# Kernel tuning notes

Hardware: AMD Instinct MI355X
Metric: run time of the kernel (lower is better)

The kernel has to match this reference:

```python
import jax, jax.numpy as jnp
import numpy as np

COMMITMENT = 0.25
THRESHOLD = 0.6
SNR_DB = 30.0  # eval_snr_db default-ish channel condition (fixed for determinism)
LN_EPS = 1e-5


def _layernorm(x, g, b):
    m = jnp.mean(x, axis=-1, keepdims=True)
    v = jnp.var(x, axis=-1, keepdims=True)
    return (x - m) * jax.lax.rsqrt(v + LN_EPS) * g + b


def _vq(x, codebook):
    # x: [T, D], codebook: [K, D]. Nearest-neighbor quantize + per-token VQ loss + STE.
    d = (x * x).sum(-1, keepdims=True) - 2.0 * (x @ codebook.T) + (codebook * codebook).sum(-1)  # [T, K]
    idx = jnp.argmin(d, axis=-1)
    q = codebook[idx]  # [T, D]
    loss = (COMMITMENT * jnp.mean((x - jax.lax.stop_gradient(q)) ** 2, axis=-1)
            + jnp.mean((jax.lax.stop_gradient(x) - q) ** 2, axis=-1))  # [T]
    q_ste = x + jax.lax.stop_gradient(q - x)
    return q_ste, loss


def setup_inputs() -> dict:
    key = jax.random.key(0)
    ks = jax.random.split(key, 8)
    B, N, De, Dq, Dd = 64, 196, 768, 512, 256
    return {
        'x_tokens': jax.random.normal(ks[0], (B, N, De), jnp.float32),
        'fim_logits': jax.random.normal(ks[1], (B, N, 1), jnp.float32),
        'W_proj': jax.random.normal(ks[2], (De, Dq), jnp.float32) * (1.0 / np.sqrt(De)),
        'b_proj': jnp.zeros((Dq,), jnp.float32),
        'ln_g': jnp.ones((Dq,), jnp.float32),
        'ln_b': jnp.zeros((Dq,), jnp.float32),
        'cb_high': jax.random.normal(ks[3], (4096, Dq), jnp.float32),
        'cb_low': jax.random.normal(ks[4], (256, Dq), jnp.float32),
        'W_dec': jax.random.normal(ks[5], (Dq, Dd), jnp.float32) * (1.0 / np.sqrt(Dq)),
        'b_dec': jnp.zeros((Dd,), jnp.float32),
        'h_ri': jax.random.normal(ks[6], (B, 2), jnp.float32),
        'noise': jax.random.normal(ks[7], (B, N, Dq), jnp.float32),
    }


def reference(x_tokens, fim_logits, W_proj, b_proj, ln_g, ln_b, cb_high, cb_low, W_dec, b_dec, h_ri, noise):
    B, N, _ = x_tokens.shape
    score = jax.nn.sigmoid(fim_logits[..., 0])          # [B, N]
    route_high = score > THRESHOLD                       # [B, N] bool

    x_proj = _layernorm(x_tokens @ W_proj + b_proj, ln_g, ln_b)  # [B, N, Dq]
    D = x_proj.shape[-1]
    xf = x_proj.reshape(-1, D)
    mf = route_high.reshape(-1)
    sf = score.reshape(-1)

    # Compute both experts densely, select with mask (same math as the masked
    # gather/scatter dispatch in the torch code, jit-friendly static shapes).
    q_high, loss_high = _vq(xf, cb_high)
    q_low, loss_low = _vq(xf, cb_low)
    final = jnp.where(mf[:, None], q_high, q_low).reshape(B, N, D)

    n_high = jnp.maximum(mf.sum(), 1)
    n_low = jnp.maximum((~mf).sum(), 1)
    vq_loss = (jnp.sum(jnp.where(mf, loss_high * sf, 0.0)) / n_high
               + jnp.sum(jnp.where(mf, 0.0, loss_low * (1.0 - sf))) / n_low) / 2.0

    # Rayleigh channel: per-sample fading magnitude h = |CN(0,1)|/sqrt(2), AWGN, equalize.
    n_var = 10.0 ** (-SNR_DB / 10.0)
    h = jnp.sqrt((h_ri ** 2).sum(-1)) / jnp.sqrt(2.0)    # [B]
    h = h[:, None, None]
    y = (h * final + jnp.sqrt(n_var) * noise) / h

    x_dec = y @ W_dec + b_dec                            # [B, N, 256]
    return x_dec, vq_loss
```

## Files before the change

kernel.cpp:

```cpp
#include <hip/hip_runtime.h>
#include <math.h>

#define T_TOK 12544
#define DE 768
#define DQ 512
#define DD 256
#define SEQ 196
#define NCH 4096
#define NCL 256
#define SPL_H 16
#define CODES_PER_BLK 256
#define MARGIN 2.0f
#define CAND_CAP 16
#define VQTOK 32

typedef __attribute__((ext_vector_type(8))) short s16x8;
typedef __attribute__((ext_vector_type(4))) float f32x4;

__device__ __forceinline__ float wave_reduce_sum(float v) {
    #pragma unroll
    for (int off = 32; off > 0; off >>= 1) v += __shfl_xor(v, off);
    return v;
}

__device__ __forceinline__ unsigned short f2bf(float f) {
    unsigned int u = __float_as_uint(f);
    u = (u + 0x7fffu + ((u >> 16) & 1u)) >> 16;
    return (unsigned short)u;
}
__device__ __forceinline__ float bf2f(unsigned short h) {
    return __uint_as_float(((unsigned int)h) << 16);
}

__device__ __forceinline__ void gload_lds16(const unsigned short* g, unsigned short* l) {
    __builtin_amdgcn_global_load_lds(
        (const __attribute__((address_space(1))) void*)g,
        (__attribute__((address_space(3))) void*)l,
        16, 0, 0);
}

__device__ __forceinline__ void sumsq_body(const float* __restrict__ cb,
                                           float* __restrict__ cs2,
                                           unsigned short* __restrict__ cbB,
                                           int blk, int NC) {
    int row = blk * 4 + (threadIdx.x >> 6);
    int lane = threadIdx.x & 63;
    if (row >= NC) return;
    const float4* p = (const float4*)(cb + (size_t)row * DQ);
    float4 a = p[lane];
    float4 b = p[lane + 64];
    if (cbB) {
        unsigned short* dst = cbB + (size_t)row * DQ;
        ushort4 ha, hb;
        ha.x = f2bf(a.x); ha.y = f2bf(a.y); ha.z = f2bf(a.z); ha.w = f2bf(a.w);
        hb.x = f2bf(b.x); hb.y = f2bf(b.y); hb.z = f2bf(b.z); hb.w = f2bf(b.w);
        *(ushort4*)(dst + lane * 4) = ha;
        *(ushort4*)(dst + 256 + lane * 4) = hb;
    }
    float s = a.x*a.x + a.y*a.y + a.z*a.z + a.w*a.w
            + b.x*b.x + b.y*b.y + b.z*b.z + b.w*b.w;
    s = wave_reduce_sum(s);
    if (lane == 0) cs2[row] = s;
}

__device__ __forceinline__ void split_body(const float* __restrict__ W, int K, int N,
                                           unsigned short* __restrict__ Thi,
                                           unsigned short* __restrict__ Tlo,
                                           int blk, int nb) {
    int total = K * N;
    for (int idx = blk * 256 + threadIdx.x; idx < total; idx += nb * 256) {
        int n = idx / K, k = idx - n * K;
        float v = W[(size_t)k * N + n];
        unsigned short h = f2bf(v);
        Thi[idx] = h;
        Tlo[idx] = f2bf(v - bf2f(h));
    }
}

__global__ __launch_bounds__(256) void prep_all(const float* __restrict__ cb_h,
                                                float* __restrict__ cs2h,
                                                unsigned short* __restrict__ cbhB,
                                                const float* __restrict__ cb_l,
                                                float* __restrict__ cs2l,
                                                unsigned short* __restrict__ cblB,
                                                const float* __restrict__ Wp,
                                                unsigned short* __restrict__ WThi,
                                                unsigned short* __restrict__ WTlo,
                                                const float* __restrict__ Wd,
                                                unsigned short* __restrict__ WdThi,
                                                unsigned short* __restrict__ WdTlo) {
    int blk = blockIdx.x;
    if (blk < 1024)       sumsq_body(cb_h, cs2h, cbhB, blk, NCH);
    else if (blk < 1088)  sumsq_body(cb_l, cs2l, cblB, blk - 1024, NCL);
    else if (blk < 1600)  split_body(Wp, DE, DQ, WThi, WTlo, blk - 1088, 512);
    else                  split_body(Wd, DQ, DD, WdThi, WdTlo, blk - 1600, 256);
}

template<int NC>
__global__ __launch_bounds__(256) void code_sumsq(const float* __restrict__ cb,
                                                  float* __restrict__ cs2) {
    sumsq_body(cb, cs2, nullptr, blockIdx.x, NC);
}

template<int KDIM, int NSTRIDE>
__global__ __launch_bounds__(256) void gemm_mfma3_128(const float* __restrict__ A,
                                                      const unsigned short* __restrict__ BThi,
                                                      const unsigned short* __restrict__ BTlo,
                                                      const float* __restrict__ bias,
                                                      float* __restrict__ out) {
    __shared__ __align__(16) unsigned short Ahi[128 * 32];
    __shared__ __align__(16) unsigned short Alo[128 * 32];
    __shared__ __align__(16) unsigned short Bhi[128 * 32];
    __shared__ __align__(16) unsigned short Blo[128 * 32];
    const int m0 = blockIdx.x * 128, n0 = blockIdx.y * 128;
    const int tid = threadIdx.x, lane = tid & 63, w = tid >> 6;
    const int wr = w >> 1, wc = w & 1;
    const int arow = tid >> 1, ahalf = tid & 1;

    const int cb0 = w * 2, cb1 = w * 2 + 1;
    const int gcol0 = n0 + cb0 * 16 + (lane >> 2);
    const int gcol1 = n0 + cb1 * 16 + (lane >> 2);
    const int ch0 = (lane & 3) ^ ((gcol0 >> 1) & 3);
    const int ch1 = (lane & 3) ^ ((gcol1 >> 1) & 3);
    const unsigned short* sH0 = BThi + (size_t)gcol0 * KDIM + ch0 * 8;
    const unsigned short* sH1 = BThi + (size_t)gcol1 * KDIM + ch1 * 8;
    const unsigned short* sL0 = BTlo + (size_t)gcol0 * KDIM + ch0 * 8;
    const unsigned short* sL1 = BTlo + (size_t)gcol1 * KDIM + ch1 * 8;

    f32x4 acc[4][4] = {};
    const int NT = KDIM / 32;
    for (int t = 0; t < NT; t++) {
        const int k0 = t * 32;
        gload_lds16(sH0 + k0, Bhi + cb0 * 512);
        gload_lds16(sH1 + k0, Bhi + cb1 * 512);
        gload_lds16(sL0 + k0, Blo + cb0 * 512);
        gload_lds16(sL1 + k0, Blo + cb1 * 512);
        {
            const float* src = A + (size_t)(m0 + arow) * KDIM + k0 + ahalf * 16;
            float4 v0 = *(const float4*)(src + 0);
            float4 v1 = *(const float4*)(src + 4);
            float4 v2 = *(const float4*)(src + 8);
            float4 v3 = *(const float4*)(src + 12);
            float xv[16] = {v0.x,v0.y,v0.z,v0.w, v1.x,v1.y,v1.z,v1.w,
                            v2.x,v2.y,v2.z,v2.w, v3.x,v3.y,v3.z,v3.w};
            const int swzA = (arow >> 1) & 3;
            #pragma unroll
            for (int cc = 0; cc < 2; cc++) {
                unsigned int hw[4], lw[4];
                #pragma unroll
                for (int j = 0; j < 4; j++) {
                    float f0 = xv[cc*8 + 2*j], f1 = xv[cc*8 + 2*j + 1];
                    unsigned short h0 = f2bf(f0), h1 = f2bf(f1);
                    unsigned short l0 = f2bf(f0 - bf2f(h0));
                    unsigned short l1 = f2bf(f1 - bf2f(h1));
                    hw[j] = (unsigned)h0 | ((unsigned)h1 << 16);
                    lw[j] = (unsigned)l0 | ((unsigned)l1 << 16);
                }
                int c = ahalf * 2 + cc;
                int doff = arow * 32 + (c ^ swzA) * 8;
                *(uint4*)&Ahi[doff] = make_uint4(hw[0], hw[1], hw[2], hw[3]);
                *(uint4*)&Alo[doff] = make_uint4(lw[0], lw[1], lw[2], lw[3]);
            }
        }
        __syncthreads();
        const int fr = lane & 15, fs = lane >> 4;
        s16x8 ah[4], al[4];
        #pragma unroll
        for (int tm = 0; tm < 4; tm++) {
            int row = wr * 64 + tm * 16 + fr;
            int off = row * 32 + (fs ^ ((row >> 1) & 3)) * 8;
            ah[tm] = *(const s16x8*)&Ahi[off];
            al[tm] = *(const s16x8*)&Alo[off];
        }
        #pragma unroll
        for (int tn = 0; tn < 4; tn++) {
            int col = wc * 64 + tn * 16 + fr;
            int boff = col * 32 + (fs ^ ((col >> 1) & 3)) * 8;
            s16x8 bh = *(const s16x8*)&Bhi[boff];
            s16x8 bl = *(const s16x8*)&Blo[boff];
            #pragma unroll
            for (int tm = 0; tm < 4; tm++) {
                acc[tm][tn] = __builtin_amdgcn_mfma_f32_16x16x32_bf16(ah[tm], bh, acc[tm][tn], 0, 0, 0);
                acc[tm][tn] = __builtin_amdgcn_mfma_f32_16x16x32_bf16(ah[tm], bl, acc[tm][tn], 0, 0, 0);
                acc[tm][tn] = __builtin_amdgcn_mfma_f32_16x16x32_bf16(al[tm], bh, acc[tm][tn], 0, 0, 0);
            }
        }
        __syncthreads();
    }
    const int fr = lane & 15, fg = lane >> 4;
    #pragma unroll
    for (int tn = 0; tn < 4; tn++) {
        const int col = n0 + wc * 64 + tn * 16 + fr;
        const float bb = bias[col];
        #pragma unroll
        for (int tm = 0; tm < 4; tm++) {
            #pragma unroll
            for (int r = 0; r < 4; r++) {
                int row = m0 + wr * 64 + tm * 16 + fg * 4 + r;
                out[(size_t)row * NSTRIDE + col] = acc[tm][tn][r] + bb;
            }
        }
    }
}

template<int KDIM, int NSTRIDE, int BN>
__global__ __launch_bounds__(256) void gemm_mfma3(const float* __restrict__ A,
                                                  const unsigned short* __restrict__ BThi,
                                                  const unsigned short* __restrict__ BTlo,
                                                  const float* __restrict__ bias,
                                                  float* __restrict__ out) {
    constexpr int CPW = BN / 64;
    __shared__ __align__(16) unsigned short Ahi[2][64 * 32];
    __shared__ __align__(16) unsigned short Alo[2][64 * 32];
    __shared__ __align__(16) unsigned short Bhi[2][BN * 32];
    __shared__ __align__(16) unsigned short Blo[2][BN * 32];
    const int m0 = blockIdx.x * 64, n0 = blockIdx.y * BN;
    const int tid = threadIdx.x, lane = tid & 63, w = tid >> 6;
    const int stok = tid >> 2, sslot = tid & 3;

    f32x4 acc[4][CPW] = {};
    float4 av0, av1;
    uint4 bh4[CPW], bl4[CPW];

    auto loadStep = [&](int k0) {
        const float* src = A + (size_t)(m0 + stok) * KDIM + k0 + sslot * 8;
        av0 = *(const float4*)src;
        av1 = *(const float4*)(src + 4);
        #pragma unroll
        for (int c = 0; c < CPW; c++) {
            size_t soff = (size_t)(n0 + c * 64 + stok) * KDIM + k0 + sslot * 8;
            bh4[c] = *(const uint4*)(BThi + soff);
            bl4[c] = *(const uint4*)(BTlo + soff);
        }
    };
    auto writeStep = [&](int buf) {
        float xv[8] = {av0.x, av0.y, av0.z, av0.w, av1.x, av1.y, av1.z, av1.w};
        unsigned int hw[4], lw[4];
        #pragma unroll
        for (int j = 0; j < 4; j++) {
            unsigned short h0 = f2bf(xv[2*j]),   h1 = f2bf(xv[2*j+1]);
            unsigned short l0 = f2bf(xv[2*j] - bf2f(h0));
            unsigned short l1 = f2bf(xv[2*j+1] - bf2f(h1));
            hw[j] = (unsigned)h0 | ((unsigned)h1 << 16);
            lw[j] = (unsigned)l0 | ((unsigned)l1 << 16);
        }
        int doffA = stok * 32 + (sslot ^ ((stok >> 1) & 3)) * 8;
        *(uint4*)&Ahi[buf][doffA] = make_uint4(hw[0], hw[1], hw[2], hw[3]);
        *(uint4*)&Alo[buf][doffA] = make_uint4(lw[0], lw[1], lw[2], lw[3]);
        #pragma unroll
        for (int c = 0; c < CPW; c++) {
            int col = c * 64 + stok;
            int doffB = col * 32 + (sslot ^ ((col >> 1) & 3)) * 8;
            *(uint4*)&Bhi[buf][doffB] = bh4[c];
            *(uint4*)&Blo[buf][doffB] = bl4[c];
        }
    };

    loadStep(0); writeStep(0); __syncthreads();
    const int NT = KDIM / 32;
    for (int t = 0; t < NT; t++) {
        const int cur = t & 1;
        if (t + 1 < NT) loadStep((t + 1) * 32);
        const int fr = lane & 15, fs = lane >> 4;
        s16x8 ah[4], al[4];
        #pragma unroll
        for (int tm = 0; tm < 4; tm++) {
            int tok = tm * 16 + fr;
            int off = tok * 32 + (fs ^ ((tok >> 1) & 3)) * 8;
            ah[tm] = *(const s16x8*)&Ahi[cur][off];
            al[tm] = *(const s16x8*)&Alo[cur][off];
        }
        #pragma unroll
        for (int n = 0; n < CPW; n++) {
            int col = w * (16 * CPW) + n * 16 + fr;
            int boff = col * 32 + (fs ^ ((col >> 1) & 3)) * 8;
            s16x8 bh = *(const s16x8*)&Bhi[cur][boff];
            s16x8 bl = *(const s16x8*)&Blo[cur][boff];
            #pragma unroll
            for (int tm = 0; tm < 4; tm++) {
                acc[tm][n] = __builtin_amdgcn_mfma_f32_16x16x32_bf16(ah[tm], bh, acc[tm][n], 0, 0, 0);
                acc[tm][n] = __builtin_amdgcn_mfma_f32_16x16x32_bf16(ah[tm], bl, acc[tm][n], 0, 0, 0);
                acc[tm][n] = __builtin_amdgcn_mfma_f32_16x16x32_bf16(al[tm], bh, acc[tm][n], 0, 0, 0);
            }
        }
        if (t + 1 < NT) writeStep(cur ^ 1);
        __syncthreads();
    }
    const int fr = lane & 15, fg = lane >> 4;
    #pragma unroll
    for (int n = 0; n < CPW; n++) {
        const int col = n0 + w * (16 * CPW) + n * 16 + fr;
        const float bb = bias[col];
        #pragma unroll
        for (int tm = 0; tm < 4; tm++) {
            #pragma unroll
            for (int r = 0; r < 4; r++) {
                int row = m0 + tm * 16 + fg * 4 + r;
                out[(size_t)row * NSTRIDE + col] = acc[tm][n][r] + bb;
            }
        }
    }
}

__global__ __launch_bounds__(256) void proj_gemm(const float* __restrict__ X,
                                                 const float* __restrict__ W,
                                                 const float* __restrict__ bias,
                                                 float* __restrict__ out) {
    __shared__ float As[32][66];
    __shared__ float Bs[32][64];
    const int m0 = blockIdx.x * 64, n0 = blockIdx.y * 64;
    const int tid = threadIdx.x;
    const int tx = tid & 15, ty = tid >> 4;
    float acc[4][4] = {};
    for (int k0 = 0; k0 < DE; k0 += 32) {
        {
            int e = tid;
            int r = e >> 3, c4 = e & 7;
            float4 v = *(const float4*)(X + (size_t)(m0 + r) * DE + k0 + c4 * 4);
            As[c4*4+0][r] = v.x; As[c4*4+1][r] = v.y; As[c4*4+2][r] = v.z; As[c4*4+3][r] = v.w;
            e = tid + 256;
            r = e >> 3; c4 = e & 7;
            v = *(const float4*)(X + (size_t)(m0 + r) * DE + k0 + c4 * 4);
            As[c4*4+0][r] = v.x; As[c4*4+1][r] = v.y; As[c4*4+2][r] = v.z; As[c4*4+3][r] = v.w;
        }
        {
            int e = tid;
            int kk = e >> 4, c4 = e & 15;
            *(float4*)&Bs[kk][c4*4] = *(const float4*)(W + (size_t)(k0 + kk) * DQ + n0 + c4 * 4);
            e = tid + 256;
            kk = e >> 4; c4 = e & 15;
            *(float4*)&Bs[kk][c4*4] = *(const float4*)(W + (size_t)(k0 + kk) * DQ + n0 + c4 * 4);
        }
        __syncthreads();
        #pragma unroll
        for (int k = 0; k < 32; k++) {
            float2 a01 = *(const float2*)&As[k][ty * 4];
            float2 a23 = *(const float2*)&As[k][ty * 4 + 2];
            float4 b = *(const float4*)&Bs[k][tx * 4];
            float av[4] = {a01.x, a01.y, a23.x, a23.y};
            float bv[4] = {b.x, b.y, b.z, b.w};
            #pragma unroll
            for (int i = 0; i < 4; i++)
                #pragma unroll
                for (int j = 0; j < 4; j++)
                    acc[i][j] += av[i] * bv[j];
        }
        __syncthreads();
    }
    float4 bv4 = *(const float4*)(bias + n0 + tx * 4);
    float bb[4] = {bv4.x, bv4.y, bv4.z, bv4.w};
    #pragma unroll
    for (int i = 0; i < 4; i++) {
        int row = m0 + ty * 4 + i;
        float4 o;
        o.x = acc[i][0] + bb[0];
        o.y = acc[i][1] + bb[1];
        o.z = acc[i][2] + bb[2];
        o.w = acc[i][3] + bb[3];
        *(float4*)(out + (size_t)row * DQ + n0 + tx * 4) = o;
    }
}

__global__ __launch_bounds__(256) void ln_route(float* __restrict__ xp,
                                                const float* __restrict__ g,
                                                const float* __restrict__ b,
                                                const float* __restrict__ logits,
                                                float* __restrict__ score,
                                                int* __restrict__ mask,
                                                unsigned short* __restrict__ xpB) {
    int row = blockIdx.x * 4 + (threadIdx.x >> 6);
    int lane = threadIdx.x & 63;
    float* p = xp + (size_t)row * DQ;
    float4 v0 = *(float4*)(p + lane * 4);
    float4 v1 = *(float4*)(p + 256 + lane * 4);
    float s  = v0.x + v0.y + v0.z + v0.w + v1.x + v1.y + v1.z + v1.w;
    float ss = v0.x*v0.x + v0.y*v0.y + v0.z*v0.z + v0.w*v0.w
             + v1.x*v1.x + v1.y*v1.y + v1.z*v1.z + v1.w*v1.w;
    s = wave_reduce_sum(s);
    ss = wave_reduce_sum(ss);
    float m = s * (1.f / DQ);
    float var = ss * (1.f / DQ) - m * m;
    float scale = rsqrtf(var + 1e-5f);
    float4 g0 = *(const float4*)(g + lane * 4);
    float4 g1 = *(const float4*)(g + 256 + lane * 4);
    float4 b0 = *(const float4*)(b + lane * 4);
    float4 b1 = *(const float4*)(b + 256 + lane * 4);
    float4 o0, o1;
    o0.x = (v0.x - m) * scale * g0.x + b0.x;
    o0.y = (v0.y - m) * scale * g0.y + b0.y;
    o0.z = (v0.z - m) * scale * g0.z + b0.z;
    o0.w = (v0.w - m) * scale * g0.w + b0.w;
    o1.x = (v1.x - m) * scale * g1.x + b1.x;
    o1.y = (v1.y - m) * scale * g1.y + b1.y;
    o1.z = (v1.z - m) * scale * g1.z + b1.z;
    o1.w = (v1.w - m) * scale * g1.w + b1.w;
    *(float4*)(p + lane * 4) = o0;
    *(float4*)(p + 256 + lane * 4) = o1;
    if (xpB) {
        unsigned short* dst = xpB + (size_t)row * DQ;
        ushort4 h0, h1;
        h0.x = f2bf(o0.x); h0.y = f2bf(o0.y); h0.z = f2bf(o0.z); h0.w = f2bf(o0.w);
        h1.x = f2bf(o1.x); h1.y = f2bf(o1.y); h1.z = f2bf(o1.z); h1.w = f2bf(o1.w);
        *(ushort4*)(dst + lane * 4) = h0;
        *(ushort4*)(dst + 256 + lane * 4) = h1;
    }
    if (lane == 0) {
        float lg = logits[row];
        float sc = 1.f / (1.f + expf(-lg));
        score[row] = sc;
        mask[row] = sc > 0.6f ? 1 : 0;
    }
}

__global__ __launch_bounds__(1024) void scan_compact(const int* __restrict__ mask,
                                                     int* __restrict__ hlist,
                                                     int* __restrict__ llist,
                                                     int* __restrict__ counts) {
    __shared__ int wsum[16];
    __shared__ int base_h, base_l;
    int tid = threadIdx.x, lane = tid & 63, wid = tid >> 6;
    if (tid == 0) { base_h = 0; base_l = 0; }
    __syncthreads();
    for (int t0 = 0; t0 < T_TOK; t0 += 1024) {
        int t = t0 + tid;
        int valid = t < T_TOK;
        int m = valid ? mask[t] : 0;
        unsigned long long bal = __ballot(m);
        int pre = __popcll(bal & ((1ull << lane) - 1ull));
        if (lane == 0) wsum[wid] = __popcll(bal);
        __syncthreads();
        int woff = 0;
        for (int w = 0; w < wid; w++) woff += wsum[w];
        int btot = 0;
        for (int w = 0; w < 16; w++) btot += wsum[w];
        int vcnt = T_TOK - t0; if (vcnt > 1024) vcnt = 1024;
        int bh = base_h, bl = base_l;
        if (valid) {
            if (m) hlist[bh + woff + pre] = t;
            else   llist[bl + (tid - (woff + pre))] = t;
        }
        __syncthreads();
        if (tid == 0) { base_h = bh + btot; base_l = bl + (vcnt - btot); }
        __syncthreads();
    }
    if (tid == 0) { counts[0] = base_h; counts[1] = base_l; }
}

__global__ __launch_bounds__(256) void vq_mfma_all(const unsigned short* __restrict__ xpB,
                                                   const unsigned short* __restrict__ cbhB,
                                                   const float* __restrict__ cs2h,
                                                   const int* __restrict__ hlist,
                                                   const unsigned short* __restrict__ cblB,
                                                   const float* __restrict__ cs2l,
                                                   const int* __restrict__ llist,
                                                   const int* __restrict__ counts,
                                                   float* __restrict__ smaxH,
                                                   int* __restrict__ scntH,
                                                   uint2* __restrict__ candH,
                                                   float* __restrict__ smaxL,
                                                   int* __restrict__ scntL,
                                                   uint2* __restrict__ candL) {
    const int by = blockIdx.y;
    const unsigned short* cbB; const float* cs2; const int* list;
    float* smax; int* scnt; uint2* cand;
    int count, slice, SPLIT;
    if (by < SPL_H) {
        cbB = cbhB; cs2 = cs2h; list = hlist; count = counts[0];
        slice = by; SPLIT = SPL_H; smax = smaxH; scnt = scntH; cand = candH;
    } else {
        cbB = cblB; cs2 = cs2l; list = llist; count = counts[1];
        slice = 0; SPLIT = 1; smax = smaxL; scnt = scntL; cand = candL;
    }
    const int base = blockIdx.x * VQTOK;
    if (base >= count) return;
    const int cbase = slice * CODES_PER_BLK;

    __shared__ __align__(16) unsigned short Abuf[VQTOK * 32];
    __shared__ __align__(16) unsigned short Bbuf[256 * 32];
    __shared__ float wmaxs[4][VQTOK];
    __shared__ float tokmax[VQTOK];
    __shared__ int ccnt[VQTOK];
    __shared__ uint2 cland[VQTOK][CAND_CAP];
    __shared__ int rows_s[VQTOK];

    const int tid = threadIdx.x;
    const int lane = tid & 63;
    const int w = tid >> 6;
    const int stok = tid >> 2, sslot = tid & 3;

    if (tid < VQTOK) {
        int tl = base + tid;
        rows_s[tid] = list[tl < count ? tl : (count - 1)];
        ccnt[tid] = 0;
    }
    __syncthreads();

    const int swz = sslot ^ ((stok >> 1) & 3);
    const unsigned short* gA  = xpB + (size_t)rows_s[stok & (VQTOK - 1)] * DQ + swz * 8;
    const unsigned short* gB0 = cbB + (size_t)(cbase + 0 * 64 + stok) * DQ + swz * 8;
    const unsigned short* gB1 = cbB + (size_t)(cbase + 1 * 64 + stok) * DQ + swz * 8;
    const unsigned short* gB2 = cbB + (size_t)(cbase + 2 * 64 + stok) * DQ + swz * 8;
    const unsigned short* gB3 = cbB + (size_t)(cbase + 3 * 64 + stok) * DQ + swz * 8;
    unsigned short* dA = Abuf + w * 512;
    unsigned short* dB = Bbuf + w * 512;

    f32x4 acc[2][4] = {};

    const int NT = DQ / 32;
    for (int t = 0; t < NT; t++) {
        const int k0 = t * 32;
        if (w < 2) gload_lds16(gA + k0, dA);
        gload_lds16(gB0 + k0, dB + 0 * 2048);
        gload_lds16(gB1 + k0, dB + 1 * 2048);
        gload_lds16(gB2 + k0, dB + 2 * 2048);
        gload_lds16(gB3 + k0, dB + 3 * 2048);
        __syncthreads();
        const int fr = lane & 15, fs = lane >> 4;
        s16x8 af[2], bf[4];
        #pragma unroll
        for (int tm = 0; tm < 2; tm++) {
            int tok = tm * 16 + fr;
            af[tm] = *(const s16x8*)&Abuf[tok * 32 + (fs ^ ((tok >> 1) & 3)) * 8];
        }
        #pragma unroll
        for (int tn = 0; tn < 4; tn++) {
            int cl = w * 64 + tn * 16 + fr;
            bf[tn] = *(const s16x8*)&Bbuf[cl * 32 + (fs ^ ((cl >> 1) & 3)) * 8];
        }
        #pragma unroll
        for (int tm = 0; tm < 2; tm++)
            #pragma unroll
            for (int tn = 0; tn < 4; tn++)
                acc[tm][tn] = __builtin_amdgcn_mfma_f32_16x16x32_bf16(af[tm], bf[tn], acc[tm][tn], 0, 0, 0);
        __syncthreads();
    }

    const int fr = lane & 15, fg = lane >> 4;
    float c2[4];
    #pragma unroll
    for (int tn = 0; tn < 4; tn++) c2[tn] = 0.5f * cs2[cbase + w * 64 + tn * 16 + fr];

    #pragma unroll
    for (int tm = 0; tm < 2; tm++) {
        #pragma unroll
        for (int r = 0; r < 4; r++) {
            float m4 = -3.0e38f;
            #pragma unroll
            for (int tn = 0; tn < 4; tn++) {
                float s = acc[tm][tn][r] - c2[tn];
                m4 = fmaxf(m4, s);
            }
            #pragma unroll
            for (int off = 1; off < 16; off <<= 1)
                m4 = fmaxf(m4, __shfl_xor(m4, off));
            if (fr == 0) wmaxs[w][tm * 16 + fg * 4 + r] = m4;
        }
    }
    __syncthreads();
    if (tid < VQTOK)
        tokmax[tid] = fmaxf(fmaxf(wmaxs[0][tid], wmaxs[1][tid]),
                            fmaxf(wmaxs[2][tid], wmaxs[3][tid]));
    __syncthreads();

    #pragma unroll
    for (int tm = 0; tm < 2; tm++) {
        #pragma unroll
        for (int r = 0; r < 4; r++) {
            int token = tm * 16 + fg * 4 + r;
            float thr = tokmax[token] - MARGIN;
            #pragma unroll
            for (int tn = 0; tn < 4; tn++) {
                float s = acc[tm][tn][r] - c2[tn];
                if (s > thr) {
                    int pos = atomicAdd(&ccnt[token], 1);
                    if (pos < CAND_CAP) {
                        uint2 cd;
                        cd.x = __float_as_uint(s);
                        cd.y = (unsigned)(cbase + w * 64 + tn * 16 + fr);
                        cland[token][pos] = cd;
                    }
                }
            }
        }
    }
    __syncthreads();

    if (tid < VQTOK) {
        int tl = base + tid;
        if (tl < count) {
            smax[(size_t)tl * SPLIT + slice] = tokmax[tid];
            scnt[(size_t)tl * SPLIT + slice] = min(ccnt[tid], CAND_CAP);
        }
    }
    for (int i = tid; i < VQTOK * CAND_CAP; i += 256) {
        int token = i >> 4, j = i & (CAND_CAP - 1);
        int tl = base + token;
        if (tl < count && j < min(ccnt[token], CAND_CAP))
            cand[((size_t)tl * SPLIT + slice) * CAND_CAP + j] = cland[token][j];
    }
}

__global__ __launch_bounds__(256) void vq_rescore_all(float* __restrict__ xp,
                                                      const float* __restrict__ cb_h,
                                                      const float* __restrict__ smaxH,
                                                      const int* __restrict__ scntH,
                                                      const uint2* __restrict__ candH,
                                                      const int* __restrict__ hlist,
                                                      const float* __restrict__ cb_l,
                                                      const float* __restrict__ smaxL,
                                                      const int* __restrict__ scntL,
                                                      const uint2* __restrict__ candL,
                                                      const int* __restrict__ llist,
                                                      const int* __restrict__ counts,
                                                      int* __restrict__ out_idx,
                                                      const float* __restrict__ noise,
                                                      const float* __restrict__ h_ri,
                                                      const float* __restrict__ score,
                                                      float* __restrict__ lh,
                                                      float* __restrict__ ll) {
    const int HB = T_TOK / 4;
    int bx = blockIdx.x;
    const float* cb; const float* smax; const int* scnt; const uint2* cand; const int* list;
    int count, SPLIT, cidx;
    if (bx < HB) {
        cb = cb_h; smax = smaxH; scnt = scntH; cand = candH; list = hlist;
        count = counts[0]; SPLIT = SPL_H; cidx = 0;
    } else {
        bx -= HB;
        cb = cb_l; smax = smaxL; scnt = scntL; cand = candL; list = llist;
        count = counts[1]; SPLIT = 1; cidx = 1;
    }
    const int wid = threadIdx.x >> 6;
    const int lane = threadIdx.x & 63;
    const int tl = bx * 4 + wid;
    if (tl >= count) return;

    float gm = -3.0e38f;
    if (lane < SPLIT) gm = smax[(size_t)tl * SPLIT + lane];
    #pragma unroll
    for (int off = 1; off < 64; off <<= 1)
        gm = fmaxf(gm, __shfl_xor(gm, off));
    const float thr = gm - MARGIN;

    const int t = list[tl];
    float xv[8];
    #pragma unroll
    for (int kk = 0; kk < 8; kk++) xv[kk] = xp[(size_t)t * DQ + lane * 8 + kk];

    double bs = -1.0e300;
    int bi = 0x7fffffff;
    for (int s = 0; s < SPLIT; s++) {
        int cn = scnt[(size_t)tl * SPLIT + s];
        for (int j = 0; j < cn; j++) {
            uint2 cd = cand[((size_t)tl * SPLIT + s) * CAND_CAP + j];
            float av = __uint_as_float(cd.x);
            if (av >= thr) {
                int code = (int)cd.y;
                const float* crow = cb + (size_t)code * DQ;
                double dot = 0.0, nrm = 0.0;
                #pragma unroll
                for (int kk = 0; kk < 8; kk++) {
                    double cv = (double)crow[lane * 8 + kk];
                    dot += (double)xv[kk] * cv;
                    nrm += cv * cv;
                }
                #pragma unroll
                for (int off = 1; off < 64; off <<= 1) {
                    dot += __shfl_xor(dot, off);
                    nrm += __shfl_xor(nrm, off);
                }
                double sc = dot - 0.5 * nrm;
                if (sc > bs || (sc == bs && code < bi)) { bs = sc; bi = code; }
            }
        }
    }
    const float* qrow = cb + (size_t)bi * DQ;
    float4 q0 = *(const float4*)(qrow + lane * 8);
    float4 q1 = *(const float4*)(qrow + lane * 8 + 4);
    const float* nz = noise + (size_t)t * DQ;
    float4 n0 = *(const float4*)(nz + lane * 8);
    float4 n1 = *(const float4*)(nz + lane * 8 + 4);
    float ds = 0.f, dx;
    dx = xv[0] - q0.x; ds += dx * dx;
    dx = xv[1] - q0.y; ds += dx * dx;
    dx = xv[2] - q0.z; ds += dx * dx;
    dx = xv[3] - q0.w; ds += dx * dx;
    dx = xv[4] - q1.x; ds += dx * dx;
    dx = xv[5] - q1.y; ds += dx * dx;
    dx = xv[6] - q1.z; ds += dx * dx;
    dx = xv[7] - q1.w; ds += dx * dx;
    ds = wave_reduce_sum(ds);
    int bbt = t / SEQ;
    float hh0 = h_ri[bbt * 2], hh1 = h_ri[bbt * 2 + 1];
    float hh = sqrtf((hh0 * hh0 + hh1 * hh1) * 0.5f);
    float cc = sqrtf(1e-3f) / hh;
    float4 y0, y1;
    y0.x = q0.x + cc * n0.x; y0.y = q0.y + cc * n0.y;
    y0.z = q0.z + cc * n0.z; y0.w = q0.w + cc * n0.w;
    y1.x = q1.x + cc * n1.x; y1.y = q1.y + cc * n1.y;
    y1.z = q1.z + cc * n1.z; y1.w = q1.w + cc * n1.w;
    *(float4*)(xp + (size_t)t * DQ + lane * 8) = y0;
    *(float4*)(xp + (size_t)t * DQ + lane * 8 + 4) = y1;
    if (lane == 0) {
        out_idx[t] = bi;
        float loss = 1.25f * ds * (1.f / DQ);
        float sc = score[t];
        if (cidx == 0) { lh[t] = loss * sc;  ll[t] = 0.f; }
        else           { lh[t] = 0.f;        ll[t] = loss * (1.f - sc); }
    }
}

template<int NC, int SPLIT>
__global__ __launch_bounds__(256) void vq_partial(const float* __restrict__ xp,
                                                  const float* __restrict__ cb,
                                                  const float* __restrict__ cs2,
                                                  const int* __restrict__ list,
                                                  const int* __restrict__ counts,
                                                  int cidx,
                                                  float* __restrict__ part_s,
                                                  int* __restrict__ part_i) {
    const int count = counts[cidx];
    const int base = blockIdx.x * 64;
    if (base >= count) return;
    const int CODES = NC / SPLIT;
    const int cbase = blockIdx.y * CODES;
    __shared__ float As[32][68];
    __shared__ float Cs[32][68];
    __shared__ int rows_s[64];
    const int tid = threadIdx.x;
    if (tid < 64) {
        int tl = base + tid;
        rows_s[tid] = list[tl < count ? tl : (count - 1)];
    }
    __syncthreads();
    const int tx = tid & 15, ty = tid >> 4;
    float best_s[4];
    int best_i[4];
    #pragma unroll
    for (int i = 0; i < 4; i++) { best_s[i] = -3.0e38f; best_i[i] = 0; }
    for (int c0 = cbase; c0 < cbase + CODES; c0 += 64) {
        float acc[4][4] = {};
        for (int k0 = 0; k0 < DQ; k0 += 32) {
            {
                int e = tid;
                int r = e >> 3, c4 = e & 7;
                float4 v = *(const float4*)(xp + (size_t)rows_s[r] * DQ + k0 + c4 * 4);
                As[c4*4+0][r] = v.x; As[c4*4+1][r] = v.y; As[c4*4+2][r] = v.z; As[c4*4+3][r] = v.w;
                e = tid + 256; r = e >> 3; c4 = e & 7;
                v = *(const float4*)(xp + (size_t)rows_s[r] * DQ + k0 + c4 * 4);
                As[c4*4+0][r] = v.x; As[c4*4+1][r] = v.y; As[c4*4+2][r] = v.z; As[c4*4+3][r] = v.w;
            }
            {
                int e = tid;
                int r = e >> 3, c4 = e & 7;
                float4 v = *(const float4*)(cb + (size_t)(c0 + r) * DQ + k0 + c4 * 4);
                Cs[c4*4+0][r] = v.x; Cs[c4*4+1][r] = v.y; Cs[c4*4+2][r] = v.z; Cs[c4*4+3][r] = v.w;
                e = tid + 256; r = e >> 3; c4 = e & 7;
                v = *(const float4*)(cb + (size_t)(c0 + r) * DQ + k0 + c4 * 4);
                Cs[c4*4+0][r] = v.x; Cs[c4*4+1][r] = v.y; Cs[c4*4+2][r] = v.z; Cs[c4*4+3][r] = v.w;
            }
            __syncthreads();
            #pragma unroll
            for (int k = 0; k < 32; k++) {
                float4 a = *(const float4*)&As[k][ty * 4];
                float4 b = *(const float4*)&Cs[k][tx * 4];
                float av[4] = {a.x, a.y, a.z, a.w};
                float bv[4] = {b.x, b.y, b.z, b.w};
                #pragma unroll
                for (int i = 0; i < 4; i++)
                    #pragma unroll
                    for (int j = 0; j < 4; j++)
                        acc[i][j] += av[i] * bv[j];
            }
            __syncthreads();
        }
        float4 c2v = *(const float4*)(cs2 + c0 + tx * 4);
        float c2[4] = {c2v.x, c2v.y, c2v.z, c2v.w};
        #pragma unroll
        for (int i = 0; i < 4; i++) {
            float s = acc[i][0] - 0.5f * c2[0];
            int bi = c0 + tx * 4;
            #pragma unroll
            for (int j = 1; j < 4; j++) {
                float sj = acc[i][j] - 0.5f * c2[j];
                if (sj > s) { s = sj; bi = c0 + tx * 4 + j; }
            }
            #pragma unroll
            for (int off = 1; off < 16; off <<= 1) {
                float os = __shfl_xor(s, off);
                int oi = __shfl_xor(bi, off);
                if (os > s || (os == s && oi < bi)) { s = os; bi = oi; }
            }
            if (s > best_s[i] || (s == best_s[i] && bi < best_i[i])) {
                best_s[i] = s; best_i[i] = bi;
            }
        }
    }
    if (tx == 0) {
        #pragma unroll
        for (int i = 0; i < 4; i++) {
            int tl = base + ty * 4 + i;
            if (tl < count) {
                part_s[(size_t)tl * SPLIT + blockIdx.y] = best_s[i];
                part_i[(size_t)tl * SPLIT + blockIdx.y] = best_i[i];
            }
        }
    }
}

template<int SPLIT>
__global__ __launch_bounds__(256) void vq_reduce(const float* __restrict__ part_s,
                                                 const int* __restrict__ part_i,
                                                 const int* __restrict__ list,
                                                 const int* __restrict__ counts,
                                                 int cidx,
                                                 int* __restrict__ out_idx) {
    int tl = blockIdx.x * 256 + threadIdx.x;
    if (tl >= counts[cidx]) return;
    float bs = part_s[(size_t)tl * SPLIT];
    int bi = part_i[(size_t)tl * SPLIT];
    #pragma unroll
    for (int s = 1; s < SPLIT; s++) {
        float v = part_s[(size_t)tl * SPLIT + s];
        int vi = part_i[(size_t)tl * SPLIT + s];
        if (v > bs || (v == bs && vi < bi)) { bs = v; bi = vi; }
    }
    out_idx[list[tl]] = bi;
}

__global__ __launch_bounds__(256) void gather_loss_y(float* __restrict__ xp,
                                                     const float* __restrict__ cb_h,
                                                     const float* __restrict__ cb_l,
                                                     const int* __restrict__ idx,
                                                     const float* __restrict__ score,
                                                     const int* __restrict__ mask,
                                                     const float* __restrict__ noise,
                                                     const float* __restrict__ h_ri,
                                                     float* __restrict__ lh,
                                                     float* __restrict__ ll) {
    int t = blockIdx.x * 4 + (threadIdx.x >> 6);
    int lane = threadIdx.x & 63;
    int m = mask[t];
    float sc = score[t];
    const float* q = (m ? cb_h : cb_l) + (size_t)idx[t] * DQ;
    float* x = xp + (size_t)t * DQ;
    const float* nz = noise + (size_t)t * DQ;
    int bb = t / SEQ;
    float h0 = h_ri[bb * 2], h1 = h_ri[bb * 2 + 1];
    float h = sqrtf((h0 * h0 + h1 * h1) * 0.5f);
    float c = sqrtf(1e-3f) / h;
    float4 xv0 = *(float4*)(x + lane * 4);
    float4 xv1 = *(float4*)(x + 256 + lane * 4);
    float4 qv0 = *(const float4*)(q + lane * 4);
    float4 qv1 = *(const float4*)(q + 256 + lane * 4);
    float4 nv0 = *(const float4*)(nz + lane * 4);
    float4 nv1 = *(const float4*)(nz + 256 + lane * 4);
    float dx, ds = 0.f;
    dx = xv0.x - qv0.x; ds += dx * dx;
    dx = xv0.y - qv0.y; ds += dx * dx;
    dx = xv0.z - qv0.z; ds += dx * dx;
    dx = xv0.w - qv0.w; ds += dx * dx;
    dx = xv1.x - qv1.x; ds += dx * dx;
    dx = xv1.y - qv1.y; ds += dx * dx;
    dx = xv1.z - qv1.z; ds += dx * dx;
    dx = xv1.w - qv1.w; ds += dx * dx;
    ds = wave_reduce_sum(ds);
    float4 y0, y1;
    y0.x = qv0.x + c * nv0.x; y0.y = qv0.y + c * nv0.y;
    y0.z = qv0.z + c * nv0.z; y0.w = qv0.w + c * nv0.w;
    y1.x = qv1.x + c * nv1.x; y1.y = qv1.y + c * nv1.y;
    y1.z = qv1.z + c * nv1.z; y1.w = qv1.w + c * nv1.w;
    *(float4*)(x + lane * 4) = y0;
    *(float4*)(x + 256 + lane * 4) = y1;
    if (lane == 0) {
        float loss = 1.25f * ds * (1.f / DQ);
        lh[t] = m ? loss * sc : 0.f;
        ll[t] = m ? 0.f : loss * (1.f - sc);
    }
}

__global__ __launch_bounds__(256) void loss_reduce(const float* __restrict__ lh,
                                                   const float* __restrict__ ll,
                                                   const int* __restrict__ counts,
                                                   float* __restrict__ out) {
    __shared__ float sh[256], sl[256];
    int tid = threadIdx.x;
    float ah = 0.f, al = 0.f;
    for (int t = tid; t < T_TOK; t += 256) { ah += lh[t]; al += ll[t]; }
    sh[tid] = ah; sl[tid] = al;
    __syncthreads();
    for (int o = 128; o > 0; o >>= 1) {
        if (tid < o) { sh[tid] += sh[tid + o]; sl[tid] += sl[tid + o]; }
        __syncthreads();
    }
    if (tid == 0) {
        int nh = counts[0];
        int nl = T_TOK - nh;
        nh = nh > 1 ? nh : 1;
        nl = nl > 1 ? nl : 1;
        out[(size_t)T_TOK * DD] = 0.5f * (sh[0] / (float)nh + sl[0] / (float)nl);
    }
}

__global__ __launch_bounds__(256) void dec_gemm(const float* __restrict__ Y,
                                                const float* __restrict__ W,
                                                const float* __restrict__ bias,
                                                float* __restrict__ out) {
    __shared__ float As[32][66];
    __shared__ float Bs[32][64];
    const int m0 = blockIdx.x * 64, n0 = blockIdx.y * 64;
    const int tid = threadIdx.x;
    const int tx = tid & 15, ty = tid >> 4;
    float acc[4][4] = {};
    for (int k0 = 0; k0 < DQ; k0 += 32) {
        {
            int e = tid;
            int r = e >> 3, c4 = e & 7;
            float4 v = *(const float4*)(Y + (size_t)(m0 + r) * DQ + k0 + c4 * 4);
            As[c4*4+0][r] = v.x; As[c4*4+1][r] = v.y; As[c4*4+2][r] = v.z; As[c4*4+3][r] = v.w;
            e = tid + 256; r = e >> 3; c4 = e & 7;
            v = *(const float4*)(Y + (size_t)(m0 + r) * DQ + k0 + c4 * 4);
            As[c4*4+0][r] = v.x; As[c4*4+1][r] = v.y; As[c4*4+2][r] = v.z; As[c4*4+3][r] = v.w;
        }
        {
            int e = tid;
            int kk = e >> 4, c4 = e & 15;
            *(float4*)&Bs[kk][c4*4] = *(const float4*)(W + (size_t)(k0 + kk) * DD + n0 + c4 * 4);
            e = tid + 256; kk = e >> 4; c4 = e & 15;
            *(float4*)&Bs[kk][c4*4] = *(const float4*)(W + (size_t)(k0 + kk) * DD + n0 + c4 * 4);
        }
        __syncthreads();
        #pragma unroll
        for (int k = 0; k < 32; k++) {
            float2 a01 = *(const float2*)&As[k][ty * 4];
            float2 a23 = *(const float2*)&As[k][ty * 4 + 2];
            float4 b = *(const float4*)&Bs[k][tx * 4];
            float av[4] = {a01.x, a01.y, a23.x, a23.y};
            float bv[4] = {b.x, b.y, b.z, b.w};
            #pragma unroll
            for (int i = 0; i < 4; i++)
                #pragma unroll
                for (int j = 0; j < 4; j++)
                    acc[i][j] += av[i] * bv[j];
        }
        __syncthreads();
    }
    float4 bv4 = *(const float4*)(bias + n0 + tx * 4);
    float bbv[4] = {bv4.x, bv4.y, bv4.z, bv4.w};
    #pragma unroll
    for (int i = 0; i < 4; i++) {
        int row = m0 + ty * 4 + i;
        float4 o;
        o.x = acc[i][0] + bbv[0];
        o.y = acc[i][1] + bbv[1];
        o.z = acc[i][2] + bbv[2];
        o.w = acc[i][3] + bbv[3];
        *(float4*)(out + (size_t)row * DD + n0 + tx * 4) = o;
    }
}

extern "C" void kernel_launch(void* const* d_in, const int* in_sizes, int n_in,
                              void* d_out, int out_size, void* d_ws, size_t ws_size,
                              hipStream_t stream) {
    const float* x_tokens = (const float*)d_in[0];
    const float* fim      = (const float*)d_in[1];
    const float* W_proj   = (const float*)d_in[2];
    const float* b_proj   = (const float*)d_in[3];
    const float* ln_g     = (const float*)d_in[4];
    const float* ln_b     = (const float*)d_in[5];
    const float* cb_high  = (const float*)d_in[6];
    const float* cb_low   = (const float*)d_in[7];
    const float* W_dec    = (const float*)d_in[8];
    const float* b_dec    = (const float*)d_in[9];
    const float* h_ri     = (const float*)d_in[10];
    const float* noise    = (const float*)d_in[11];
    float* out = (float*)d_out;

    char* ws = (char*)d_ws;
    size_t off = 0;
    float* xp = (float*)(ws + off);     off += (size_t)T_TOK * DQ * 4;
    int*   idxb = (int*)(ws + off);     off += (size_t)T_TOK * 4;
    float* score = (float*)(ws + off);  off += (size_t)T_TOK * 4;
    int*   mask = (int*)(ws + off);     off += (size_t)T_TOK * 4;
    float* lh = (float*)(ws + off);     off += (size_t)T_TOK * 4;
    float* ll = (float*)(ws + off);     off += (size_t)T_TOK * 4;
    int*   hlist = (int*)(ws + off);    off += (size_t)T_TOK * 4;
    int*   llist = (int*)(ws + off);    off += (size_t)T_TOK * 4;
    int*   counts = (int*)(ws + off);   off += 64;
    float* cs2h = (float*)(ws + off);   off += (size_t)NCH * 4;
    float* cs2l = (float*)(ws + off);   off += (size_t)NCL * 4;
    size_t off_common = off;

    unsigned short* xpB  = (unsigned short*)(ws + off); off += (size_t)T_TOK * DQ * 2;
    unsigned short* cbhB = (unsigned short*)(ws + off); off += (size_t)NCH * DQ * 2;
    unsigned short* cblB = (unsigned short*)(ws + off); off += (size_t)NCL * DQ * 2;
    float* smaxH = (float*)(ws + off);  off += (size_t)T_TOK * SPL_H * 4;
    int*   scntH = (int*)(ws + off);    off += (size_t)T_TOK * SPL_H * 4;
    uint2* candH = (uint2*)(ws + off);  off += (size_t)T_TOK * SPL_H * CAND_CAP * 8;
    float* smaxL = (float*)(ws + off);  off += (size_t)T_TOK * 4;
    int*   scntL = (int*)(ws + off);    off += (size_t)T_TOK * 4;
    uint2* candL = (uint2*)(ws + off);  off += (size_t)T_TOK * CAND_CAP * 8;
    unsigned short* WThi  = (unsigned short*)(ws + off); off += (size_t)DQ * DE * 2;
    unsigned short* WTlo  = (unsigned short*)(ws + off); off += (size_t)DQ * DE * 2;
    unsigned short* WdThi = (unsigned short*)(ws + off); off += (size_t)DD * DQ * 2;
    unsigned short* WdTlo = (unsigned short*)(ws + off); off += (size_t)DD * DQ * 2;
    size_t need_new = off;
    const bool use_mfma = ws_size >= need_new;

    if (use_mfma) {
        prep_all<<<1856, 256, 0, stream>>>(cb_high, cs2h, cbhB, cb_low, cs2l, cblB,
                                           W_proj, WThi, WTlo, W_dec, WdThi, WdTlo);
        gemm_mfma3_128<DE, DQ><<<dim3(T_TOK / 128, DQ / 128), 256, 0, stream>>>(
            x_tokens, WThi, WTlo, b_proj, xp);
        ln_route<<<T_TOK / 4, 256, 0, stream>>>(xp, ln_g, ln_b, fim, score, mask, xpB);
        scan_compact<<<1, 1024, 0, stream>>>(mask, hlist, llist, counts);
        vq_mfma_all<<<dim3(T_TOK / VQTOK, SPL_H + 1), 256, 0, stream>>>(
            xpB, cbhB, cs2h, hlist, cblB, cs2l, llist, counts,
            smaxH, scntH, candH, smaxL, scntL, candL);
        vq_rescore_all<<<2 * (T_TOK / 4), 256, 0, stream>>>(
            xp, cb_high, smaxH, scntH, candH, hlist,
            cb_low, smaxL, scntL, candL, llist,
            counts, idxb, noise, h_ri, score, lh, ll);
        loss_reduce<<<1, 256, 0, stream>>>(lh, ll, counts, out);
        gemm_mfma3<DQ, DD, 64><<<dim3(T_TOK / 64, DD / 64), 256, 0, stream>>>(
            xp, WdThi, WdTlo, b_dec, out);
    } else {
        code_sumsq<NCH><<<NCH / 4, 256, 0, stream>>>(cb_high, cs2h);
        code_sumsq<NCL><<<NCL / 4, 256, 0, stream>>>(cb_low, cs2l);
        proj_gemm<<<dim3(T_TOK / 64, DQ / 64), 256, 0, stream>>>(x_tokens, W_proj, b_proj, xp);
        ln_route<<<T_TOK / 4, 256, 0, stream>>>(xp, ln_g, ln_b, fim, score, mask, nullptr);
        scan_compact<<<1, 1024, 0, stream>>>(mask, hlist, llist, counts);
        float* part_s = (float*)(ws + off_common);
        int*   part_i = (int*)(ws + off_common + (size_t)T_TOK * 16 * 4);
        vq_partial<NCH, 16><<<dim3(T_TOK / 64, 16), 256, 0, stream>>>(
            xp, cb_high, cs2h, hlist, counts, 0, part_s, part_i);
        vq_reduce<16><<<(T_TOK + 255) / 256, 256, 0, stream>>>(part_s, part_i, hlist, counts, 0, idxb);
        vq_partial<NCL, 4><<<dim3(T_TOK / 64, 4), 256, 0, stream>>>(
            xp, cb_low, cs2l, llist, counts, 1, part_s, part_i);
        vq_reduce<4><<<(T_TOK + 255) / 256, 256, 0, stream>>>(part_s, part_i, llist, counts, 1, idxb);
        gather_loss_y<<<T_TOK / 4, 256, 0, stream>>>(xp, cb_high, cb_low, idxb, score, mask,
                                                     noise, h_ri, lh, ll);
        loss_reduce<<<1, 256, 0, stream>>>(lh, ll, counts, out);
        dec_gemm<<<dim3(T_TOK / 64, DD / 64), 256, 0, stream>>>(xp, W_dec, b_dec, out);
    }
}
```

Measured before the change: 211.7 us.

## Fuse routing compaction into layernorm and loss reduction into decoder GEMM

Replaces the separate ln_route and single-block scan_compact kernels with one kernel that normalizes rows and appends token indices to the high and low lists through shared-memory and global atomics. The counters are zeroed inside prep_all. The final loss_reduce launch is folded into the decoder GEMM as an extra block column, which removes two launches and a serial single-block scan. In exchange, list order is no longer deterministic, so tie-breaking and downstream ordering may change.

```diff
diff --git a/kernel.cpp b/kernel.cpp
--- a/kernel.cpp
+++ b/kernel.cpp
@@ -88,8 +88,10 @@
                                                 unsigned short* __restrict__ WTlo,
                                                 const float* __restrict__ Wd,
                                                 unsigned short* __restrict__ WdThi,
-                                                unsigned short* __restrict__ WdTlo) {
+                                                unsigned short* __restrict__ WdTlo,
+                                                int* __restrict__ counts) {
     int blk = blockIdx.x;
+    if (blk == 0 && threadIdx.x == 0) { counts[0] = 0; counts[1] = 0; }
     if (blk < 1024)       sumsq_body(cb_h, cs2h, cbhB, blk, NCH);
     else if (blk < 1088)  sumsq_body(cb_l, cs2l, cblB, blk - 1024, NCL);
     else if (blk < 1600)  split_body(Wp, DE, DQ, WThi, WTlo, blk - 1088, 512);
@@ -203,35 +205,55 @@
     }
 }
 
-template<int KDIM, int NSTRIDE, int BN>
-__global__ __launch_bounds__(256) void gemm_mfma3(const float* __restrict__ A,
-                                                  const unsigned short* __restrict__ BThi,
-                                                  const unsigned short* __restrict__ BTlo,
-                                                  const float* __restrict__ bias,
-                                                  float* __restrict__ out) {
-    constexpr int CPW = BN / 64;
+__global__ __launch_bounds__(256) void dec_mfma3_loss(const float* __restrict__ A,
+                                                      const unsigned short* __restrict__ BThi,
+                                                      const unsigned short* __restrict__ BTlo,
+                                                      const float* __restrict__ bias,
+                                                      float* __restrict__ out,
+                                                      const float* __restrict__ lh,
+                                                      const float* __restrict__ ll,
+                                                      const int* __restrict__ counts) {
     __shared__ __align__(16) unsigned short Ahi[2][64 * 32];
     __shared__ __align__(16) unsigned short Alo[2][64 * 32];
-    __shared__ __align__(16) unsigned short Bhi[2][BN * 32];
-    __shared__ __align__(16) unsigned short Blo[2][BN * 32];
-    const int m0 = blockIdx.x * 64, n0 = blockIdx.y * BN;
+    __shared__ __align__(16) unsigned short Bhi[2][64 * 32];
+    __shared__ __align__(16) unsigned short Blo[2][64 * 32];
+    if (blockIdx.x == T_TOK / 64) {
+        if (blockIdx.y != 0) return;
+        float* sh = (float*)&Ahi[0][0];
+        float* sl = sh + 256;
+        int tid = threadIdx.x;
+        float ah = 0.f, al = 0.f;
+        for (int t = tid; t < T_TOK; t += 256) { ah += lh[t]; al += ll[t]; }
+        sh[tid] = ah; sl[tid] = al;
+        __syncthreads();
+        for (int o = 128; o > 0; o >>= 1) {
+            if (tid < o) { sh[tid] += sh[tid + o]; sl[tid] += sl[tid + o]; }
+            __syncthreads();
+        }
+        if (tid == 0) {
+            int nh = counts[0];
+            int nl = T_TOK - nh;
+            nh = nh > 1 ? nh : 1;
+            nl = nl > 1 ? nl : 1;
+            out[(size_t)T_TOK * DD] = 0.5f * (sh[0] / (float)nh + sl[0] / (float)nl);
+        }
+        return;
+    }
+    const int m0 = blockIdx.x * 64, n0 = blockIdx.y * 64;
     const int tid = threadIdx.x, lane = tid & 63, w = tid >> 6;
     const int stok = tid >> 2, sslot = tid & 3;
 
-    f32x4 acc[4][CPW] = {};
+    f32x4 acc[4] = {};
     float4 av0, av1;
-    uint4 bh4[CPW], bl4[CPW];
+    uint4 bh4, bl4;
 
     auto loadStep = [&](int k0) {
-        const float* src = A + (size_t)(m0 + stok) * KDIM + k0 + sslot * 8;
+        const float* src = A + (size_t)(m0 + stok) * DQ + k0 + sslot * 8;
         av0 = *(const float4*)src;
         av1 = *(const float4*)(src + 4);
-        #pragma unroll
-        for (int c = 0; c < CPW; c++) {
-            size_t soff = (size_t)(n0 + c * 64 + stok) * KDIM + k0 + sslot * 8;
-            bh4[c] = *(const uint4*)(BThi + soff);
-            bl4[c] = *(const uint4*)(BTlo + soff);
-        }
+        size_t soff = (size_t)(n0 + stok) * DQ + k0 + sslot * 8;
+        bh4 = *(const uint4*)(BThi + soff);
+        bl4 = *(const uint4*)(BTlo + soff);
     };
     auto writeStep = [&](int buf) {
         float xv[8] = {av0.x, av0.y, av0.z, av0.w, av1.x, av1.y, av1.z, av1.w};
@@ -247,17 +269,12 @@
         int doffA = stok * 32 + (sslot ^ ((stok >> 1) & 3)) * 8;
         *(uint4*)&Ahi[buf][doffA] = make_uint4(hw[0], hw[1], hw[2], hw[3]);
         *(uint4*)&Alo[buf][doffA] = make_uint4(lw[0], lw[1], lw[2], lw[3]);
-        #pragma unroll
-        for (int c = 0; c < CPW; c++) {
-            int col = c * 64 + stok;
-            int doffB = col * 32 + (sslot ^ ((col >> 1) & 3)) * 8;
-            *(uint4*)&Bhi[buf][doffB] = bh4[c];
-            *(uint4*)&Blo[buf][doffB] = bl4[c];
-        }
+        *(uint4*)&Bhi[buf][doffA] = bh4;
+        *(uint4*)&Blo[buf][doffA] = bl4;
     };
 
     loadStep(0); writeStep(0); __syncthreads();
-    const int NT = KDIM / 32;
+    const int NT = DQ / 32;
     for (int t = 0; t < NT; t++) {
         const int cur = t & 1;
         if (t + 1 < NT) loadStep((t + 1) * 32);
@@ -270,33 +287,31 @@
             ah[tm] = *(const s16x8*)&Ahi[cur][off];
             al[tm] = *(const s16x8*)&Alo[cur][off];
         }
-        #pragma unroll
-        for (int n = 0; n < CPW; n++) {
-            int col = w * (16 * CPW) + n * 16 + fr;
+        {
+            int col = w * 16 + fr;
             int boff = col * 32 + (fs ^ ((col >> 1) & 3)) * 8;
             s16x8 bh = *(const s16x8*)&Bhi[cur][boff];
             s16x8 bl = *(const s16x8*)&Blo[cur][boff];
             #pragma unroll
             for (int tm = 0; tm < 4; tm++) {
-                acc[tm][n] = __builtin_amdgcn_mfma_f32_16x16x32_bf16(ah[tm], bh, acc[tm][n], 0, 0, 0);
-                acc[tm][n] = __builtin_amdgcn_mfma_f32_16x16x32_bf16(ah[tm], bl, acc[tm][n], 0, 0, 0);
-                acc[tm][n] = __builtin_amdgcn_mfma_f32_16x16x32_bf16(al[tm], bh, acc[tm][n], 0, 0, 0);
+                acc[tm] = __builtin_amdgcn_mfma_f32_16x16x32_bf16(ah[tm], bh, acc[tm], 0, 0, 0);
+                acc[tm] = __builtin_amdgcn_mfma_f32_16x16x32_bf16(ah[tm], bl, acc[tm], 0, 0, 0);
+                acc[tm] = __builtin_amdgcn_mfma_f32_16x16x32_bf16(al[tm], bh, acc[tm], 0, 0, 0);
             }
         }
         if (t + 1 < NT) writeStep(cur ^ 1);
         __syncthreads();
     }
     const int fr = lane & 15, fg = lane >> 4;
-    #pragma unroll
-    for (int n = 0; n < CPW; n++) {
-        const int col = n0 + w * (16 * CPW) + n * 16 + fr;
+    {
+        const int col = n0 + w * 16 + fr;
         const float bb = bias[col];
         #pragma unroll
         for (int tm = 0; tm < 4; tm++) {
             #pragma unroll
             for (int r = 0; r < 4; r++) {
                 int row = m0 + tm * 16 + fg * 4 + r;
-                out[(size_t)row * NSTRIDE + col] = acc[tm][n][r] + bb;
+                out[(size_t)row * DD + col] = acc[tm][r] + bb;
             }
         }
     }
@@ -358,6 +373,77 @@
         o.z = acc[i][2] + bb[2];
         o.w = acc[i][3] + bb[3];
         *(float4*)(out + (size_t)row * DQ + n0 + tx * 4) = o;
+    }
+}
+
+__global__ __launch_bounds__(256) void ln_route_compact(float* __restrict__ xp,
+                                                        const float* __restrict__ g,
+                                                        const float* __restrict__ b,
+                                                        const float* __restrict__ logits,
+                                                        float* __restrict__ score,
+                                                        unsigned short* __restrict__ xpB,
+                                                        int* __restrict__ hlist,
+                                                        int* __restrict__ llist,
+                                                        int* __restrict__ counts) {
+    __shared__ int hloc[32], lloc[32];
+    __shared__ int nh_s, nl_s, bh_s, bl_s;
+    const int tid = threadIdx.x, lane = tid & 63, wv = tid >> 6;
+    if (tid == 0) { nh_s = 0; nl_s = 0; }
+    __syncthreads();
+    float4 g0 = *(const float4*)(g + lane * 4);
+    float4 g1 = *(const float4*)(g + 256 + lane * 4);
+    float4 b0 = *(const float4*)(b + lane * 4);
+    float4 b1 = *(const float4*)(b + 256 + lane * 4);
+    const int rbase = blockIdx.x * 32 + wv * 8;
+    for (int i = 0; i < 8; i++) {
+        int row = rbase + i;
+        float* p = xp + (size_t)row * DQ;
+        float4 v0 = *(float4*)(p + lane * 4);
+        float4 v1 = *(float4*)(p + 256 + lane * 4);
+        float s  = v0.x + v0.y + v0.z + v0.w + v1.x + v1.y + v1.z + v1.w;
+        float ss = v0.x*v0.x + v0.y*v0.y + v0.z*v0.z + v0.w*v0.w
+                 + v1.x*v1.x + v1.y*v1.y + v1.z*v1.z + v1.w*v1.w;
+        s = wave_reduce_sum(s);
+        ss = wave_reduce_sum(ss);
+        float m = s * (1.f / DQ);
+        float var = ss * (1.f / DQ) - m * m;
+        float scale = rsqrtf(var + 1e-5f);
+        float4 o0, o1;
+        o0.x = (v0.x - m) * scale * g0.x + b0.x;
+        o0.y = (v0.y - m) * scale * g0.y + b0.y;
+        o0.z = (v0.z - m) * scale * g0.z + b0.z;
+        o0.w = (v0.w - m) * scale * g0.w + b0.w;
+        o1.x = (v1.x - m) * scale * g1.x + b1.x;
+        o1.y = (v1.y - m) * scale * g1.y + b1.y;
+        o1.z = (v1.z - m) * scale * g1.z + b1.z;
+        o1.w = (v1.w - m) * scale * g1.w + b1.w;
+        *(float4*)(p + lane * 4) = o0;
+        *(float4*)(p + 256 + lane * 4) = o1;
+        unsigned short* dst = xpB + (size_t)row * DQ;
+        ushort4 h0, h1;
+        h0.x = f2bf(o0.x); h0.y = f2bf(o0.y); h0.z = f2bf(o0.z); h0.w = f2bf(o0.w);
+        h1.x = f2bf(o1.x); h1.y = f2bf(o1.y); h1.z = f2bf(o1.z); h1.w = f2bf(o1.w);
+        *(ushort4*)(dst + lane * 4) = h0;
+        *(ushort4*)(dst + 256 + lane * 4) = h1;
+        if (lane == 0) {
+            float lg = logits[row];
+            float sc = 1.f / (1.f + expf(-lg));
+            score[row] = sc;
+            if (sc > 0.6f) { int pp = atomicAdd(&nh_s, 1); hloc[pp] = row; }
+            else           { int pp = atomicAdd(&nl_s, 1); lloc[pp] = row; }
+        }
+    }
+    __syncthreads();
+    if (tid == 0) {
+        bh_s = atomicAdd(&counts[0], nh_s);
+        bl_s = atomicAdd(&counts[1], nl_s);
+    }
+    __syncthreads();
+    if (tid < 32) {
+        if (tid < nh_s) hlist[bh_s + tid] = hloc[tid];
+    } else if (tid < 64) {
+        int j = tid - 32;
+        if (j < nl_s) llist[bl_s + j] = lloc[j];
     }
 }
 
@@ -1009,11 +1095,11 @@
 
     if (use_mfma) {
         prep_all<<<1856, 256, 0, stream>>>(cb_high, cs2h, cbhB, cb_low, cs2l, cblB,
-                                           W_proj, WThi, WTlo, W_dec, WdThi, WdTlo);
+                                           W_proj, WThi, WTlo, W_dec, WdThi, WdTlo, counts);
         gemm_mfma3_128<DE, DQ><<<dim3(T_TOK / 128, DQ / 128), 256, 0, stream>>>(
             x_tokens, WThi, WTlo, b_proj, xp);
-        ln_route<<<T_TOK / 4, 256, 0, stream>>>(xp, ln_g, ln_b, fim, score, mask, xpB);
-        scan_compact<<<1, 1024, 0, stream>>>(mask, hlist, llist, counts);
+        ln_route_compact<<<T_TOK / 32, 256, 0, stream>>>(
+            xp, ln_g, ln_b, fim, score, xpB, hlist, llist, counts);
         vq_mfma_all<<<dim3(T_TOK / VQTOK, SPL_H + 1), 256, 0, stream>>>(
             xpB, cbhB, cs2h, hlist, cblB, cs2l, llist, counts,
             smaxH, scntH, candH, smaxL, scntL, candL);
@@ -1021,9 +1107,8 @@
             xp, cb_high, smaxH, scntH, candH, hlist,
             cb_low, smaxL, scntL, candL, llist,
             counts, idxb, noise, h_ri, score, lh, ll);
-        loss_reduce<<<1, 256, 0, stream>>>(lh, ll, counts, out);
-        gemm_mfma3<DQ, DD, 64><<<dim3(T_TOK / 64, DD / 64), 256, 0, stream>>>(
-            xp, WdThi, WdTlo, b_dec, out);
+        dec_mfma3_loss<<<dim3(T_TOK / 64 + 1, DD / 64), 256, 0, stream>>>(
+            xp, WdThi, WdTlo, b_dec, out, lh, ll, counts);
     } else {
         code_sumsq<NCH><<<NCH / 4, 256, 0, stream>>>(cb_high, cs2h);
         code_sumsq<NCL><<<NCL / 4, 256, 0, stream>>>(cb_low, cs2l);
```

New measurement: 198.4 us. -6.3%, faster.
